# Kernel optimization log

Measured on AMD Instinct MI355X. Metric: run time of the kernel, lower is better.

## Reference

```python
import jax, jax.numpy as jnp
import numpy as np


def setup_inputs() -> dict:
    key = jax.random.key(0)
    T, B, D, R = 1024, 32, 1024, 256
    ks = jax.random.split(key, 6)
    scale = 1.0 / np.sqrt(D)
    x = jax.random.normal(ks[0], (T, B, D), dtype=jnp.float32)
    h0 = jnp.zeros((B, D), dtype=jnp.float32)
    W_alpha = jax.random.normal(ks[1], (D, D), dtype=jnp.float32) * scale
    b_alpha = jnp.full((D,), 2.0, dtype=jnp.float32)  # init_alpha_bias
    U = jax.random.normal(ks[2], (D, R), dtype=jnp.float32) * (0.5 / np.sqrt(R))
    V = jax.random.normal(ks[3], (R, D), dtype=jnp.float32) * (0.5 * scale)
    W_x = jax.random.normal(ks[4], (D, D), dtype=jnp.float32) * scale
    b = jnp.zeros((D,), dtype=jnp.float32)
    return {"x": x, "h0": h0, "W_alpha": W_alpha, "b_alpha": b_alpha,
            "U": U, "V": V, "W_x": W_x, "b": b}


def reference(x, h0, W_alpha, b_alpha, U, V, W_x, b):
    # Precompute input projections for all timesteps (as in the torch fallback)
    alpha_x_all = jnp.einsum('tbd,ed->tbe', x, W_alpha) + b_alpha  # [T,B,D]
    Wx_all = jnp.einsum('tbd,ed->tbe', x, W_x) + b                 # [T,B,D]

    def step(h_prev, inp):
        ax, wx = inp
        alpha = jax.nn.sigmoid(ax)                       # retain gate
        v = jnp.tanh((h_prev @ V.T) @ U.T + wx)          # low-rank h mixing
        h_new = alpha * h_prev + (1.0 - alpha) * v
        out = h_new * jax.nn.silu(h_new)
        return h_new, (h_new, out)

    _, (h_seq, output) = jax.lax.scan(step, h0, (alpha_x_all, Wx_all))
    h = jnp.concatenate([h0[None], h_seq], axis=0)       # [T+1,B,D]
    return output, h
```

## Files before the change

### kernel.cpp

```cpp
#include <hip/hip_runtime.h>

typedef _Float16 f16;
typedef f16 f16x2 __attribute__((ext_vector_type(2)));
typedef f16 f16x8 __attribute__((ext_vector_type(8)));
typedef float f32x4 __attribute__((ext_vector_type(4)));

#define TT 1024
#define BB 32
#define DD 1024
#define RR 256

__device__ __forceinline__ float dot2f(f16x2 a, f16x2 b, float c) {
#if __has_builtin(__builtin_amdgcn_fdot2)
    return __builtin_amdgcn_fdot2(a, b, c, false);
#else
    return c + (float)a[0] * (float)b[0] + (float)a[1] * (float)b[1];
#endif
}

__device__ __forceinline__ float sigm_f(float x) { return 1.0f / (1.0f + __expf(-x)); }
__device__ __forceinline__ float tanh_f(float x) { return 1.0f - 2.0f / (1.0f + __expf(2.0f * x)); }

__global__ __launch_bounds__(256)
void fused_pregemm(const float* __restrict__ X, const float* __restrict__ Wa,
                   const float* __restrict__ Wx, const float* __restrict__ ba,
                   const float* __restrict__ bb, f16* __restrict__ axo,
                   f16* __restrict__ wxo)
{
    __shared__ __align__(16) f16 lA[64][40];
    __shared__ __align__(16) f16 lB[64][40];
    __shared__ __align__(16) f16 lC[64][40];

    const int tid = threadIdx.x;
    const int w   = tid >> 6;
    const int l   = tid & 63;
    const int la  = l & 15;
    const int qd  = l >> 4;
    const int m0  = blockIdx.x * 64;
    const int n0  = blockIdx.y * 64;
    const int sr  = tid >> 2;
    const int sk  = (tid & 3) * 8;

    f32x4 accA[4] = {};
    f32x4 accX[4] = {};

    for (int k0 = 0; k0 < DD; k0 += 32) {
        {
            const float* pX = X + (size_t)(m0 + sr) * DD + k0 + sk;
            float4 v0 = *(const float4*)pX;
            float4 v1 = *(const float4*)(pX + 4);
            f16x8 x8 = {(f16)v0.x, (f16)v0.y, (f16)v0.z, (f16)v0.w,
                        (f16)v1.x, (f16)v1.y, (f16)v1.z, (f16)v1.w};
            *(f16x8*)&lA[sr][sk] = x8;

            const float* pA = Wa + (size_t)(n0 + sr) * DD + k0 + sk;
            v0 = *(const float4*)pA;
            v1 = *(const float4*)(pA + 4);
            f16x8 a8 = {(f16)v0.x, (f16)v0.y, (f16)v0.z, (f16)v0.w,
                        (f16)v1.x, (f16)v1.y, (f16)v1.z, (f16)v1.w};
            *(f16x8*)&lB[sr][sk] = a8;

            const float* pW = Wx + (size_t)(n0 + sr) * DD + k0 + sk;
            v0 = *(const float4*)pW;
            v1 = *(const float4*)(pW + 4);
            f16x8 w8 = {(f16)v0.x, (f16)v0.y, (f16)v0.z, (f16)v0.w,
                        (f16)v1.x, (f16)v1.y, (f16)v1.z, (f16)v1.w};
            *(f16x8*)&lC[sr][sk] = w8;
        }
        __syncthreads();

        f16x8 af = *(const f16x8*)&lA[16 * w + la][qd * 8];
        #pragma unroll
        for (int c = 0; c < 4; c++) {
            f16x8 b1 = *(const f16x8*)&lB[16 * c + la][qd * 8];
            f16x8 b2 = *(const f16x8*)&lC[16 * c + la][qd * 8];
            accA[c] = __builtin_amdgcn_mfma_f32_16x16x32_f16(af, b1, accA[c], 0, 0, 0);
            accX[c] = __builtin_amdgcn_mfma_f32_16x16x32_f16(af, b2, accX[c], 0, 0, 0);
        }
        __syncthreads();
    }

    #pragma unroll
    for (int c = 0; c < 4; c++) {
        const int n = n0 + 16 * c + la;
        const float bav = ba[n];
        const float bbv = bb[n];
        #pragma unroll
        for (int r = 0; r < 4; r++) {
            const int m = m0 + 16 * w + qd * 4 + r;
            axo[(size_t)m * DD + n] = (f16)(accA[c][r] + bav);
            wxo[(size_t)m * DD + n] = (f16)(accX[c][r] + bbv);
        }
    }
}

__global__ __launch_bounds__(1024, 4)
void rnn_scan(const f16* __restrict__ ax, const f16* __restrict__ wx,
              const float* __restrict__ V, const float* __restrict__ U,
              const float* __restrict__ h0, float* __restrict__ out,
              float* __restrict__ hout)
{
    const int b   = blockIdx.x;
    const int tid = threadIdx.x;
    const int s   = tid >> 6;
    const int q   = tid & 63;
    const int e2  = tid >> 1;
    const int z   = tid & 1;

    __shared__ __align__(16) f16 h2[DD];
    __shared__ float hf[DD];
    __shared__ float part[16][RR];
    __shared__ __align__(16) f16 pl[RR];
    __shared__ float up[DD][2];

    f16x2 wv[4][32];
    #pragma unroll
    for (int j = 0; j < 4; j++) {
        const float2* vr = (const float2*)(V + (size_t)(4 * q + j) * DD + 64 * s);
        #pragma unroll
        for (int i = 0; i < 32; i++) {
            float2 t = vr[i];
            f16x2 p2 = {(f16)t.x, (f16)t.y};
            wv[j][i] = p2;
        }
    }
    f16x2 wu[2][64];
    #pragma unroll
    for (int j = 0; j < 2; j++) {
        const float2* ur = (const float2*)(U + (size_t)(2 * e2 + j) * RR + 128 * z);
        #pragma unroll
        for (int i = 0; i < 64; i++) {
            float2 t = ur[i];
            f16x2 p2 = {(f16)t.x, (f16)t.y};
            wu[j][i] = p2;
        }
    }

    const float h0v = h0[(size_t)b * DD + tid];
    hf[tid] = h0v;
    h2[tid] = (f16)h0v;
    hout[(size_t)b * DD + tid] = h0v;

    const f16* axp  = ax  + (size_t)b * DD + tid;
    const f16* wxp  = wx  + (size_t)b * DD + tid;
    float*     outp = out + (size_t)b * DD + tid;
    float*     houtp = hout + (size_t)BB * DD + (size_t)b * DD + tid;

    __syncthreads();

    #pragma unroll 1
    for (int t = 0; t < TT; t++) {
        const f16x8* hsl = (const f16x8*)(h2 + 64 * s);
        float acc[4] = {0.f, 0.f, 0.f, 0.f};
        #pragma unroll
        for (int i = 0; i < 8; i++) {
            f16x8 hv = hsl[i];
            f16x2 hp[4];
            hp[0][0] = hv[0]; hp[0][1] = hv[1];
            hp[1][0] = hv[2]; hp[1][1] = hv[3];
            hp[2][0] = hv[4]; hp[2][1] = hv[5];
            hp[3][0] = hv[6]; hp[3][1] = hv[7];
            #pragma unroll
            for (int u = 0; u < 4; u++) {
                #pragma unroll
                for (int j = 0; j < 4; j++) {
                    acc[j] = dot2f(wv[j][4 * i + u], hp[u], acc[j]);
                }
            }
        }
        part[s][4 * q + 0] = acc[0];
        part[s][4 * q + 1] = acc[1];
        part[s][4 * q + 2] = acc[2];
        part[s][4 * q + 3] = acc[3];
        __syncthreads();

        if (tid < RR) {
            float pv = 0.f;
            #pragma unroll
            for (int ss = 0; ss < 16; ss++) pv += part[ss][tid];
            pl[tid] = (f16)pv;
        }
        __syncthreads();

        const f16x8* psl = (const f16x8*)(pl + 128 * z);
        float ua[2] = {0.f, 0.f};
        #pragma unroll
        for (int i = 0; i < 16; i++) {
            f16x8 pv8 = psl[i];
            f16x2 pp[4];
            pp[0][0] = pv8[0]; pp[0][1] = pv8[1];
            pp[1][0] = pv8[2]; pp[1][1] = pv8[3];
            pp[2][0] = pv8[4]; pp[2][1] = pv8[5];
            pp[3][0] = pv8[6]; pp[3][1] = pv8[7];
            #pragma unroll
            for (int u = 0; u < 4; u++) {
                ua[0] = dot2f(wu[0][4 * i + u], pp[u], ua[0]);
                ua[1] = dot2f(wu[1][4 * i + u], pp[u], ua[1]);
            }
        }
        up[2 * e2 + 0][z] = ua[0];
        up[2 * e2 + 1][z] = ua[1];
        __syncthreads();

        {
            float uu = up[tid][0] + up[tid][1] + (float)*wxp;
            float vv = tanh_f(uu);
            float aa = sigm_f((float)*axp);
            float hp = hf[tid];
            float hn = aa * hp + (1.0f - aa) * vv;
            float so = hn * hn * sigm_f(hn);
            *outp  = so;
            *houtp = hn;
            hf[tid] = hn;
            h2[tid] = (f16)hn;
            axp += BB * DD; wxp += BB * DD; outp += BB * DD; houtp += BB * DD;
        }
        __syncthreads();
    }
}

extern "C" void kernel_launch(void* const* d_in, const int* in_sizes, int n_in,
                              void* d_out, int out_size, void* d_ws, size_t ws_size,
                              hipStream_t stream) {
    (void)in_sizes; (void)n_in; (void)out_size; (void)ws_size;
    const float* x  = (const float*)d_in[0];
    const float* h0 = (const float*)d_in[1];
    const float* Wa = (const float*)d_in[2];
    const float* ba = (const float*)d_in[3];
    const float* U  = (const float*)d_in[4];
    const float* V  = (const float*)d_in[5];
    const float* Wx = (const float*)d_in[6];
    const float* bb = (const float*)d_in[7];

    float* out  = (float*)d_out;
    float* hout = out + (size_t)TT * BB * DD;

    f16* ax16 = (f16*)d_ws;
    f16* wx16 = ax16 + (size_t)TT * BB * DD;

    dim3 g1(512, 16);
    fused_pregemm<<<g1, dim3(256), 0, stream>>>(x, Wa, Wx, ba, bb, ax16, wx16);
    rnn_scan<<<dim3(BB), dim3(1024), 0, stream>>>(ax16, wx16, V, U, h0, out, hout);
}
```

Baseline: 16.64 ms.

## Split each batch row's scan across four workgroups with global flag synchronization

The recurrent scan for each batch element is divided across four workgroups, each owning a quarter of the low-rank dimension R. Each workgroup computes a partial U·(V·h) product, publishes it to a global double-buffered exchange buffer, and spin-waits on per-workgroup release/acquire flags before summing all partials and updating the full hidden state redundantly. The goal is to cut per-step register/ALU work per workgroup and use more CUs (128 instead of 32). The cost is a cross-workgroup global-memory handshake every timestep, which adds latency, and the spin-waits can deadlock unless all 128 workgroups are resident at the same time.

```diff
diff --git a/kernel.cpp b/kernel.cpp
--- a/kernel.cpp
+++ b/kernel.cpp
@@ -9,6 +9,8 @@
 #define BB 32
 #define DD 1024
 #define RR 256
+#define QR 64
+#define NQ 4
 
 __device__ __forceinline__ float dot2f(f16x2 a, f16x2 b, float c) {
 #if __has_builtin(__builtin_amdgcn_fdot2)
@@ -94,87 +96,86 @@
     }
 }
 
+__global__ void zero_flags(unsigned* __restrict__ flags) {
+    flags[threadIdx.x] = 0;
+}
+
 __global__ __launch_bounds__(1024, 4)
-void rnn_scan(const f16* __restrict__ ax, const f16* __restrict__ wx,
-              const float* __restrict__ V, const float* __restrict__ U,
-              const float* __restrict__ h0, float* __restrict__ out,
-              float* __restrict__ hout)
+void rnn_scan4(const f16* __restrict__ ax, const f16* __restrict__ wx,
+               const float* __restrict__ V, const float* __restrict__ U,
+               const float* __restrict__ h0, float* __restrict__ out,
+               float* __restrict__ hout, float* __restrict__ ubuf,
+               unsigned* __restrict__ flags)
 {
-    const int b   = blockIdx.x;
+    const int w   = blockIdx.x;
+    const int b   = w >> 2;
+    const int q   = w & 3;
+    const int b4  = b << 2;
     const int tid = threadIdx.x;
-    const int s   = tid >> 6;
-    const int q   = tid & 63;
-    const int e2  = tid >> 1;
-    const int z   = tid & 1;
+    const int rl  = tid & 63;
+    const int ds  = tid >> 6;
 
     __shared__ __align__(16) f16 h2[DD];
     __shared__ float hf[DD];
-    __shared__ float part[16][RR];
-    __shared__ __align__(16) f16 pl[RR];
-    __shared__ float up[DD][2];
-
-    f16x2 wv[4][32];
-    #pragma unroll
-    for (int j = 0; j < 4; j++) {
-        const float2* vr = (const float2*)(V + (size_t)(4 * q + j) * DD + 64 * s);
+    __shared__ float part[16][QR];
+    __shared__ __align__(16) f16 pl[QR];
+
+    f16x2 wv1[32];
+    {
+        const float2* vp = (const float2*)(V + (size_t)(q * QR + rl) * DD + ds * 64);
         #pragma unroll
         for (int i = 0; i < 32; i++) {
-            float2 t = vr[i];
-            f16x2 p2 = {(f16)t.x, (f16)t.y};
-            wv[j][i] = p2;
-        }
-    }
-    f16x2 wu[2][64];
-    #pragma unroll
-    for (int j = 0; j < 2; j++) {
-        const float2* ur = (const float2*)(U + (size_t)(2 * e2 + j) * RR + 128 * z);
-        #pragma unroll
-        for (int i = 0; i < 64; i++) {
-            float2 t = ur[i];
-            f16x2 p2 = {(f16)t.x, (f16)t.y};
-            wu[j][i] = p2;
+            float2 tv = vp[i];
+            f16x2 p2 = {(f16)tv.x, (f16)tv.y};
+            wv1[i] = p2;
+        }
+    }
+    f16x2 wu1[32];
+    {
+        const float2* up2 = (const float2*)(U + (size_t)tid * RR + q * QR);
+        #pragma unroll
+        for (int i = 0; i < 32; i++) {
+            float2 tu = up2[i];
+            f16x2 p2 = {(f16)tu.x, (f16)tu.y};
+            wu1[i] = p2;
         }
     }
 
     const float h0v = h0[(size_t)b * DD + tid];
     hf[tid] = h0v;
     h2[tid] = (f16)h0v;
-    hout[(size_t)b * DD + tid] = h0v;
-
-    const f16* axp  = ax  + (size_t)b * DD + tid;
-    const f16* wxp  = wx  + (size_t)b * DD + tid;
-    float*     outp = out + (size_t)b * DD + tid;
+    if ((tid >> 8) == q) hout[(size_t)b * DD + tid] = h0v;
+
+    const f16* axp   = ax  + (size_t)b * DD + tid;
+    const f16* wxp   = wx  + (size_t)b * DD + tid;
+    float*     outp  = out + (size_t)b * DD + tid;
     float*     houtp = hout + (size_t)BB * DD + (size_t)b * DD + tid;
+
+    float* myu = ubuf + ((size_t)w * 2) * 1024;
 
     __syncthreads();
 
     #pragma unroll 1
     for (int t = 0; t < TT; t++) {
-        const f16x8* hsl = (const f16x8*)(h2 + 64 * s);
-        float acc[4] = {0.f, 0.f, 0.f, 0.f};
+        const float axv = (float)*axp;
+        const float wxv = (float)*wxp;
+
+        const f16x8* hsl = (const f16x8*)(h2 + ds * 64);
+        float acc = 0.f;
         #pragma unroll
         for (int i = 0; i < 8; i++) {
             f16x8 hv = hsl[i];
-            f16x2 hp[4];
-            hp[0][0] = hv[0]; hp[0][1] = hv[1];
-            hp[1][0] = hv[2]; hp[1][1] = hv[3];
-            hp[2][0] = hv[4]; hp[2][1] = hv[5];
-            hp[3][0] = hv[6]; hp[3][1] = hv[7];
-            #pragma unroll
-            for (int u = 0; u < 4; u++) {
-                #pragma unroll
-                for (int j = 0; j < 4; j++) {
-                    acc[j] = dot2f(wv[j][4 * i + u], hp[u], acc[j]);
-                }
-            }
-        }
-        part[s][4 * q + 0] = acc[0];
-        part[s][4 * q + 1] = acc[1];
-        part[s][4 * q + 2] = acc[2];
-        part[s][4 * q + 3] = acc[3];
-        __syncthreads();
-
-        if (tid < RR) {
+            f16x2 hp0 = {hv[0], hv[1]}, hp1 = {hv[2], hv[3]};
+            f16x2 hp2 = {hv[4], hv[5]}, hp3 = {hv[6], hv[7]};
+            acc = dot2f(wv1[4 * i + 0], hp0, acc);
+            acc = dot2f(wv1[4 * i + 1], hp1, acc);
+            acc = dot2f(wv1[4 * i + 2], hp2, acc);
+            acc = dot2f(wv1[4 * i + 3], hp3, acc);
+        }
+        part[ds][rl] = acc;
+        __syncthreads();
+
+        if (tid < QR) {
             float pv = 0.f;
             #pragma unroll
             for (int ss = 0; ss < 16; ss++) pv += part[ss][tid];
@@ -182,39 +183,57 @@
         }
         __syncthreads();
 
-        const f16x8* psl = (const f16x8*)(pl + 128 * z);
-        float ua[2] = {0.f, 0.f};
-        #pragma unroll
-        for (int i = 0; i < 16; i++) {
+        const f16x8* psl = (const f16x8*)pl;
+        float ua = 0.f;
+        #pragma unroll
+        for (int i = 0; i < 8; i++) {
             f16x8 pv8 = psl[i];
-            f16x2 pp[4];
-            pp[0][0] = pv8[0]; pp[0][1] = pv8[1];
-            pp[1][0] = pv8[2]; pp[1][1] = pv8[3];
-            pp[2][0] = pv8[4]; pp[2][1] = pv8[5];
-            pp[3][0] = pv8[6]; pp[3][1] = pv8[7];
-            #pragma unroll
-            for (int u = 0; u < 4; u++) {
-                ua[0] = dot2f(wu[0][4 * i + u], pp[u], ua[0]);
-                ua[1] = dot2f(wu[1][4 * i + u], pp[u], ua[1]);
+            f16x2 pp0 = {pv8[0], pv8[1]}, pp1 = {pv8[2], pv8[3]};
+            f16x2 pp2 = {pv8[4], pv8[5]}, pp3 = {pv8[6], pv8[7]};
+            ua = dot2f(wu1[4 * i + 0], pp0, ua);
+            ua = dot2f(wu1[4 * i + 1], pp1, ua);
+            ua = dot2f(wu1[4 * i + 2], pp2, ua);
+            ua = dot2f(wu1[4 * i + 3], pp3, ua);
+        }
+
+        const int slot = t & 1;
+        myu[slot * 1024 + tid] = ua;
+        __syncthreads();
+        if (tid == 0)
+            __hip_atomic_store(&flags[w], (unsigned)(t + 1),
+                               __ATOMIC_RELEASE, __HIP_MEMORY_SCOPE_AGENT);
+
+        const unsigned need = (unsigned)(t + 1);
+        #pragma unroll
+        for (int j = 1; j < NQ; j++) {
+            const int pw = b4 + ((q + j) & 3);
+            if ((tid & 63) == 0) {
+                while (__hip_atomic_load(&flags[pw], __ATOMIC_ACQUIRE,
+                                         __HIP_MEMORY_SCOPE_AGENT) < need)
+                    __builtin_amdgcn_s_sleep(1);
             }
         }
-        up[2 * e2 + 0][z] = ua[0];
-        up[2 * e2 + 1][z] = ua[1];
-        __syncthreads();
-
+
+        float ut = ua;
+        #pragma unroll
+        for (int j = 1; j < NQ; j++) {
+            const int pw = b4 + ((q + j) & 3);
+            ut += ubuf[((size_t)pw * 2 + slot) * 1024 + tid];
+        }
         {
-            float uu = up[tid][0] + up[tid][1] + (float)*wxp;
-            float vv = tanh_f(uu);
-            float aa = sigm_f((float)*axp);
-            float hp = hf[tid];
-            float hn = aa * hp + (1.0f - aa) * vv;
-            float so = hn * hn * sigm_f(hn);
-            *outp  = so;
-            *houtp = hn;
+            const float uu = ut + wxv;
+            const float vv = tanh_f(uu);
+            const float aa = sigm_f(axv);
+            const float hp = hf[tid];
+            const float hn = aa * hp + (1.0f - aa) * vv;
             hf[tid] = hn;
             h2[tid] = (f16)hn;
-            axp += BB * DD; wxp += BB * DD; outp += BB * DD; houtp += BB * DD;
-        }
+            if ((tid >> 8) == q) {
+                *outp  = hn * hn * sigm_f(hn);
+                *houtp = hn;
+            }
+        }
+        axp += BB * DD; wxp += BB * DD; outp += BB * DD; houtp += BB * DD;
         __syncthreads();
     }
 }
@@ -237,8 +256,12 @@
 
     f16* ax16 = (f16*)d_ws;
     f16* wx16 = ax16 + (size_t)TT * BB * DD;
+    float* ubuf = (float*)(wx16 + (size_t)TT * BB * DD);
+    unsigned* flags = (unsigned*)(ubuf + (size_t)BB * NQ * 2 * 1024);
 
     dim3 g1(512, 16);
     fused_pregemm<<<g1, dim3(256), 0, stream>>>(x, Wa, Wx, ba, bb, ax16, wx16);
-    rnn_scan<<<dim3(BB), dim3(1024), 0, stream>>>(ax16, wx16, V, U, h0, out, hout);
-}
+    zero_flags<<<dim3(1), dim3(BB * NQ), 0, stream>>>(flags);
+    rnn_scan4<<<dim3(BB * NQ), dim3(1024), 0, stream>>>(ax16, wx16, V, U, h0,
+                                                        out, hout, ubuf, flags);
+}
```

New measurement: 60.23 ms. 3.62x slower.
